# Performance work log

Hardware: AMD Instinct MI355X
Metric: run time of the kernel (lower is better)

The kernel has to match this reference:

```python
import jax, jax.numpy as jnp
import numpy as np

B, N, D = 8, 1024, 512
H = 8
DH = D // H
EPS_DIST = 1e-8
EPS_LN = 1e-5


def _layer_norm(x, gamma, beta):
    mu = jnp.mean(x, axis=-1, keepdims=True)
    var = jnp.mean((x - mu) ** 2, axis=-1, keepdims=True)
    return (x - mu) * jax.lax.rsqrt(var + EPS_LN) * gamma + beta


def setup_inputs() -> dict:
    key = jax.random.key(0)
    ks = jax.random.split(key, 6)
    scale = 1.0 / np.sqrt(D)
    inp = {
        "x": jax.random.normal(ks[0], (B, N, D), dtype=jnp.float32),
        "Wq": jax.random.normal(ks[1], (D, D), dtype=jnp.float32) * scale,
        "Wk": jax.random.normal(ks[2], (D, D), dtype=jnp.float32) * scale,
        "Wv": jax.random.normal(ks[3], (D, D), dtype=jnp.float32) * scale,
        "Wo": jax.random.normal(ks[4], (D, D), dtype=jnp.float32) * scale,
        "bq": jnp.zeros((D,), jnp.float32),
        "bk": jnp.zeros((D,), jnp.float32),
        "bv": jnp.zeros((D,), jnp.float32),
        "bo": jnp.zeros((D,), jnp.float32),
        "ln1_g": jnp.ones((D,), jnp.float32),
        "ln1_b": jnp.zeros((D,), jnp.float32),
        "ln2_g": jnp.ones((D,), jnp.float32),
        "ln2_b": jnp.zeros((D,), jnp.float32),
    }
    return inp


def reference(x, Wq, bq, Wk, bk, Wv, bv, Wo, bo, ln1_g, ln1_b, ln2_g, ln2_b):
    residual = x
    h = _layer_norm(x, ln1_g, ln1_b)  # pre-norm

    def heads(t):
        # [B,N,D] -> [B,H,N,DH]
        return t.reshape(B, N, H, DH).transpose(0, 2, 1, 3)

    q = heads(h @ Wq + bq)
    k = heads(h @ Wk + bk)
    v = heads(h @ Wv + bv)

    # Euclidean pairwise distance via ||q||^2 + ||k||^2 - 2 q.k expansion
    q_sq = jnp.sum(q * q, axis=-1)[..., :, None]      # [B,H,N,1]
    k_sq = jnp.sum(k * k, axis=-1)[..., None, :]      # [B,H,1,N]
    qk = jnp.einsum("bhnd,bhmd->bhnm", q, k)          # [B,H,N,N]
    d2 = jnp.maximum(q_sq + k_sq - 2.0 * qk, 0.0)
    dist = jnp.sqrt(d2 + EPS_DIST)

    # distance -> attention score: smaller distance = higher attention
    attn = jax.nn.softmax(-dist, axis=-1)             # [B,H,N,N]

    out = jnp.einsum("bhnm,bhmd->bhnd", attn, v)      # [B,H,N,DH]
    out = out.transpose(0, 2, 1, 3).reshape(B, N, D)
    out = out @ Wo + bo

    y = residual + out
    y = _layer_norm(y, ln2_g, ln2_b)
    return y
```

## Files before the change

kernel.cpp:

```cpp
#include <hip/hip_runtime.h>
#include <math.h>

typedef __attribute__((ext_vector_type(8))) short short8;
typedef __attribute__((ext_vector_type(4))) float f32x4;

constexpr int B  = 8;
constexpr int N  = 1024;
constexpr int D  = 512;
constexpr int H  = 8;
constexpr int DH = 64;
constexpr int M_ROWS = 8192;
constexpr float EPS_DIST = 1e-8f;
constexpr float EPS_LN   = 1e-5f;

__device__ inline unsigned short bfbits(float f) {
    union { float f; unsigned u; } v; v.f = f;
    unsigned r = v.u + 0x7fffu + ((v.u >> 16) & 1u);
    return (unsigned short)(r >> 16);
}
__device__ inline float bf2f(unsigned short s) {
    union { unsigned u; float f; } v; v.u = ((unsigned)s) << 16; return v.f;
}

__device__ inline int swz(int row) {
    return (((row >> 2) & 3) << 4) ^ ((row & 3) << 3);
}

__device__ inline void async_ld16(unsigned short* lds, const unsigned short* g) {
    __builtin_amdgcn_global_load_lds(
        (const __attribute__((address_space(1))) unsigned int*)(g),
        (__attribute__((address_space(3))) unsigned int*)(lds),
        16, 0, 0);
}

__device__ inline float block_sum256(float s, float* red) {
    for (int o = 32; o > 0; o >>= 1) s += __shfl_down(s, o, 64);
    int lane = threadIdx.x & 63, wid = threadIdx.x >> 6;
    if (lane == 0) red[wid] = s;
    __syncthreads();
    if (threadIdx.x == 0) red[4] = red[0] + red[1] + red[2] + red[3];
    __syncthreads();
    return red[4];
}

__global__ __launch_bounds__(256) void prep_kernel(const float* __restrict__ Wq,
                                                   const float* __restrict__ Wk,
                                                   const float* __restrict__ Wv,
                                                   const float* __restrict__ Wo,
                                                   unsigned short* __restrict__ WtAll,
                                                   const float* __restrict__ x,
                                                   const float* __restrict__ ln1_g,
                                                   const float* __restrict__ ln1_b,
                                                   unsigned short* __restrict__ h_bf) {
    __shared__ float red[8];
    const int bxg = blockIdx.x;
    if (bxg < 256) {
        int sub = bxg >> 6;
        const float* W = sub == 0 ? Wq : sub == 1 ? Wk : sub == 2 ? Wv : Wo;
        unsigned short* Wt = WtAll + (size_t)sub * 262144;
        int t = (bxg & 63) * 256 + threadIdx.x;
        int tn = t & 127, tk = t >> 7;
        int k = tk * 4, n = tn * 4;
        float4 r0 = *(const float4*)&W[(size_t)(k + 0) * 512 + n];
        float4 r1 = *(const float4*)&W[(size_t)(k + 1) * 512 + n];
        float4 r2 = *(const float4*)&W[(size_t)(k + 2) * 512 + n];
        float4 r3 = *(const float4*)&W[(size_t)(k + 3) * 512 + n];
        ushort4 c;
        c.x = bfbits(r0.x); c.y = bfbits(r1.x); c.z = bfbits(r2.x); c.w = bfbits(r3.x);
        *(ushort4*)&Wt[(size_t)(n + 0) * 512 + k] = c;
        c.x = bfbits(r0.y); c.y = bfbits(r1.y); c.z = bfbits(r2.y); c.w = bfbits(r3.y);
        *(ushort4*)&Wt[(size_t)(n + 1) * 512 + k] = c;
        c.x = bfbits(r0.z); c.y = bfbits(r1.z); c.z = bfbits(r2.z); c.w = bfbits(r3.z);
        *(ushort4*)&Wt[(size_t)(n + 2) * 512 + k] = c;
        c.x = bfbits(r0.w); c.y = bfbits(r1.w); c.z = bfbits(r2.w); c.w = bfbits(r3.w);
        *(ushort4*)&Wt[(size_t)(n + 3) * 512 + k] = c;
    } else {
        const int row = bxg - 256;
        const int t = threadIdx.x;
        const float* xr = x + (size_t)row * D;
        float v0 = xr[t], v1 = xr[t + 256];
        float mu = block_sum256(v0 + v1, red) * (1.0f / D);
        float d0 = v0 - mu, d1 = v1 - mu;
        float var = block_sum256(d0 * d0 + d1 * d1, red) * (1.0f / D);
        float rstd = rsqrtf(var + EPS_LN);
        h_bf[(size_t)row * D + t]       = bfbits(d0 * rstd * ln1_g[t] + ln1_b[t]);
        h_bf[(size_t)row * D + t + 256] = bfbits(d1 * rstd * ln1_g[t + 256] + ln1_b[t + 256]);
    }
}

__global__ __launch_bounds__(256) void ln2_kernel(const unsigned short* __restrict__ y0,
                                                  const float* __restrict__ res,
                                                  const float* __restrict__ gamma,
                                                  const float* __restrict__ beta,
                                                  float* __restrict__ out) {
    __shared__ float red[8];
    const int row = blockIdx.x;
    const int t = threadIdx.x;
    const unsigned short* xr = y0 + (size_t)row * D;
    const float* rr = res + (size_t)row * D;
    float v0 = bf2f(xr[t]) + rr[t];
    float v1 = bf2f(xr[t + 256]) + rr[t + 256];
    float mu = block_sum256(v0 + v1, red) * (1.0f / D);
    float d0 = v0 - mu, d1 = v1 - mu;
    float var = block_sum256(d0 * d0 + d1 * d1, red) * (1.0f / D);
    float rstd = rsqrtf(var + EPS_LN);
    out[(size_t)row * D + t]       = d0 * rstd * gamma[t] + beta[t];
    out[(size_t)row * D + t + 256] = d1 * rstd * gamma[t + 256] + beta[t + 256];
}

template <int MT>
__global__ __launch_bounds__(256) void gemm_qkv(const unsigned short* __restrict__ A,
                                                const unsigned short* __restrict__ Wt,
                                                const float* __restrict__ bias0,
                                                const float* __restrict__ bias1,
                                                const float* __restrict__ bias2,
                                                unsigned short* __restrict__ Qo,
                                                unsigned short* __restrict__ Ko,
                                                unsigned short* __restrict__ Vo,
                                                float* __restrict__ sq0,
                                                float* __restrict__ sq1) {
    constexpr int RB = M_ROWS / MT;
    constexpr int NI = MT / 32;
    constexpr int ASZ = MT * 64, BSZ = 128 * 64;
    constexpr int SMSZ = (ASZ + BSZ > 18432) ? ASZ + BSZ : 18432;
    __shared__ unsigned short smem[SMSZ];
    unsigned short* As = smem;
    unsigned short* Bs = smem + ASZ;

    const int id = blockIdx.x;
    const int by = id & (RB - 1), bx = id / RB;
    const int tid = threadIdx.x;
    const int lane = tid & 63, wv = tid >> 6;
    const int quad = lane >> 4, l15 = lane & 15;
    const int row0 = by * MT, col0 = bx * 128;
    const int wm = (wv & 1) * (MT / 2), wn = (wv >> 1) * 64;

    f32x4 acc[NI][4];
    #pragma unroll
    for (int i = 0; i < NI; ++i)
        #pragma unroll
        for (int j = 0; j < 4; ++j) acc[i][j] = (f32x4){0.f, 0.f, 0.f, 0.f};

    const unsigned short* Ag = A  + (size_t)row0 * 512;
    const unsigned short* Bg = Wt + (size_t)col0 * 512;

    for (int k0 = 0; k0 < 512; k0 += 64) {
        __syncthreads();
        #pragma unroll
        for (int c = 0; c < ASZ / 2048; ++c) {
            int fu = c * 2048 + tid * 8;
            int r = fu >> 6, ko = fu & 63;
            async_ld16(As + fu, Ag + (size_t)r * 512 + k0 + ko);
        }
        #pragma unroll
        for (int c = 0; c < BSZ / 2048; ++c) {
            int fu = c * 2048 + tid * 8;
            int r = fu >> 6, ko = fu & 63;
            async_ld16(Bs + fu, Bg + (size_t)r * 512 + k0 + ko);
        }
        __syncthreads();

        #pragma unroll
        for (int ks = 0; ks < 2; ++ks) {
            short8 af[NI], bf[4];
            #pragma unroll
            for (int i = 0; i < NI; ++i)
                af[i] = *(const short8*)&As[(wm + i * 16 + l15) * 64 + ks * 32 + quad * 8];
            #pragma unroll
            for (int j = 0; j < 4; ++j)
                bf[j] = *(const short8*)&Bs[(wn + j * 16 + l15) * 64 + ks * 32 + quad * 8];
            #pragma unroll
            for (int i = 0; i < NI; ++i)
                #pragma unroll
                for (int j = 0; j < 4; ++j)
                    acc[i][j] = __builtin_amdgcn_mfma_f32_16x16x32_bf16(af[i], bf[j], acc[i][j], 0, 0, 0);
        }
    }

    const int colg = col0 + wn;
    const int seg = colg >> 9;
    const int hh = (colg & 511) >> 6;
    const float* bias = seg == 0 ? bias0 : seg == 1 ? bias1 : bias2;

    if (seg < 2) {
        unsigned short* dst = seg == 0 ? Qo : Ko;
        float* sq = seg == 0 ? sq0 : sq1;
        #pragma unroll
        for (int i = 0; i < NI; ++i) {
            const int m0 = row0 + wm + i * 16 + quad * 4;
            float ss[4] = {0.f, 0.f, 0.f, 0.f};
            #pragma unroll
            for (int j = 0; j < 4; ++j) {
                float bvj = bias[hh * 64 + j * 16 + l15];
                #pragma unroll
                for (int r = 0; r < 4; ++r) {
                    float v = acc[i][j][r] + bvj;
                    unsigned short ub = bfbits(v);
                    float vr = bf2f(ub);
                    ss[r] += vr * vr;
                    int m = m0 + r;
                    int b_ = m >> 10, n_ = m & 1023;
                    dst[((size_t)((b_ * 8 + hh) * 1024) + n_) * 64 + j * 16 + l15] = ub;
                }
            }
            #pragma unroll
            for (int r = 0; r < 4; ++r) {
                float s = ss[r];
                s += __shfl_xor(s, 1, 64);
                s += __shfl_xor(s, 2, 64);
                s += __shfl_xor(s, 4, 64);
                s += __shfl_xor(s, 8, 64);
                if (l15 == 0) {
                    int m = m0 + r;
                    sq[(size_t)((m >> 10) * 8 + hh) * 1024 + (m & 1023)] = s;
                }
            }
        }
    } else {
        __syncthreads();
        unsigned short* T = smem + wv * 4608;
        #pragma unroll
        for (int i = 0; i < NI; ++i)
            #pragma unroll
            for (int j = 0; j < 4; ++j) {
                float bvj = bias[hh * 64 + j * 16 + l15];
                ushort4 pk;
                pk.x = bfbits(acc[i][j][0] + bvj);
                pk.y = bfbits(acc[i][j][1] + bvj);
                pk.z = bfbits(acc[i][j][2] + bvj);
                pk.w = bfbits(acc[i][j][3] + bvj);
                *(ushort4*)&T[(j * 16 + l15) * 72 + i * 16 + quad * 4] = pk;
            }
        const int b_ = (row0 + wm) >> 10;
        const int nbase = (row0 + wm) & 1023;
        unsigned short* Vg = Vo + ((size_t)((b_ * 8 + hh) * 64)) * 1024 + nbase;
        #pragma unroll
        for (int it = 0; it < 8; ++it) {
            int dl = it * 8 + (lane >> 3);
            int nl = (lane & 7) * 8;
            uint4 v = *(const uint4*)&T[dl * 72 + nl];
            *(uint4*)&Vg[(size_t)dl * 1024 + nl] = v;
        }
    }
}

__global__ __launch_bounds__(256) void gemm_out(const unsigned short* __restrict__ A,
                                                const unsigned short* __restrict__ Wt,
                                                const float* __restrict__ bias,
                                                unsigned short* __restrict__ C) {
    __shared__ unsigned short As[64 * 64];
    __shared__ unsigned short Bs[128 * 64];

    const int id = blockIdx.x;
    const int by = id & 127, bx = id >> 7;
    const int tid = threadIdx.x;
    const int lane = tid & 63, wv = tid >> 6;
    const int quad = lane >> 4, l15 = lane & 15;
    const int row0 = by * 64, col0 = bx * 128;
    const int wm = (wv & 1) * 32, wn = (wv >> 1) * 64;

    f32x4 acc[2][4];
    #pragma unroll
    for (int i = 0; i < 2; ++i)
        #pragma unroll
        for (int j = 0; j < 4; ++j) acc[i][j] = (f32x4){0.f, 0.f, 0.f, 0.f};

    const unsigned short* Ag = A  + (size_t)row0 * 512;
    const unsigned short* Bg = Wt + (size_t)col0 * 512;

    for (int k0 = 0; k0 < 512; k0 += 64) {
        __syncthreads();
        #pragma unroll
        for (int c = 0; c < 2; ++c) {
            int fu = c * 2048 + tid * 8;
            int r = fu >> 6, ko = fu & 63;
            async_ld16(As + fu, Ag + (size_t)r * 512 + k0 + ko);
        }
        #pragma unroll
        for (int c = 0; c < 4; ++c) {
            int fu = c * 2048 + tid * 8;
            int r = fu >> 6, ko = fu & 63;
            async_ld16(Bs + fu, Bg + (size_t)r * 512 + k0 + ko);
        }
        __syncthreads();

        #pragma unroll
        for (int ks = 0; ks < 2; ++ks) {
            short8 af[2], bf[4];
            #pragma unroll
            for (int i = 0; i < 2; ++i)
                af[i] = *(const short8*)&As[(wm + i * 16 + l15) * 64 + ks * 32 + quad * 8];
            #pragma unroll
            for (int j = 0; j < 4; ++j)
                bf[j] = *(const short8*)&Bs[(wn + j * 16 + l15) * 64 + ks * 32 + quad * 8];
            #pragma unroll
            for (int i = 0; i < 2; ++i)
                #pragma unroll
                for (int j = 0; j < 4; ++j)
                    acc[i][j] = __builtin_amdgcn_mfma_f32_16x16x32_bf16(af[i], bf[j], acc[i][j], 0, 0, 0);
        }
    }

    #pragma unroll
    for (int i = 0; i < 2; ++i)
        #pragma unroll
        for (int j = 0; j < 4; ++j) {
            int col = col0 + wn + j * 16 + l15;
            float bv = bias[col];
            #pragma unroll
            for (int r = 0; r < 4; ++r) {
                int row = row0 + wm + i * 16 + quad * 4 + r;
                C[(size_t)row * 512 + col] = bfbits(acc[i][j][r] + bv);
            }
        }
}

__global__ __launch_bounds__(512) void attn_kernel(const unsigned short* __restrict__ Q,
                                                   const unsigned short* __restrict__ K,
                                                   const unsigned short* __restrict__ Vt,
                                                   const float* __restrict__ qsq,
                                                   const float* __restrict__ ksq,
                                                   unsigned short* __restrict__ O) {
    __shared__ unsigned short Ks[2][64 * 64];
    __shared__ unsigned short Vs[2][64 * 64];
    __shared__ unsigned short Ps[8][16 * 64];
    __shared__ float ksq_s[2][64];

    const int id = blockIdx.x;
    const int bh = id & 63, qb = id >> 6;
    const int q0 = qb * 128;
    const int tid = threadIdx.x;
    const int lane = tid & 63, w = tid >> 6;
    const int quad = lane >> 4, l15 = lane & 15;
    const int b_ = bh >> 3, h_ = bh & 7;

    const unsigned short* Qb = Q  + (size_t)bh * N * DH;
    const unsigned short* Kb = K  + (size_t)bh * N * DH;
    const unsigned short* Vb = Vt + (size_t)bh * DH * N;

    short8 qf0, qf1;
    {
        const unsigned short* qp = Qb + (size_t)(q0 + w * 16 + l15) * 64 + quad * 8;
        qf0 = *(const short8*)qp;
        qf1 = *(const short8*)(qp + 32);
    }
    float qe[4];
    #pragma unroll
    for (int r = 0; r < 4; ++r)
        qe[r] = qsq[bh * N + q0 + w * 16 + quad * 4 + r] + EPS_DIST;

    f32x4 oacc[4];
    #pragma unroll
    for (int dt = 0; dt < 4; ++dt) oacc[dt] = (f32x4){0.f, 0.f, 0.f, 0.f};
    float dpart[4] = {};

    const int rr = tid >> 3;
    const int scol = ((tid & 7) * 8) ^ swz(rr);
    uint4 kreg, vreg;
    float ksreg = 0.f;

    kreg = *(const uint4*)(Kb + (size_t)rr * 64 + (tid & 7) * 8);
    vreg = *(const uint4*)(Vb + (size_t)rr * N + (tid & 7) * 8);
    if (tid < 64) ksreg = ksq[bh * N + tid];

    *(uint4*)&Ks[0][rr * 64 + scol] = kreg;
    *(uint4*)&Vs[0][rr * 64 + scol] = vreg;
    if (tid < 64) ksq_s[0][tid] = ksreg;
    __syncthreads();

    const int sR = swz(l15);

    #pragma unroll 2
    for (int kt = 0; kt < 16; ++kt) {
        const int cur = kt & 1;
        if (kt < 15) {
            kreg = *(const uint4*)(Kb + (size_t)((kt + 1) * 64 + rr) * 64 + (tid & 7) * 8);
            vreg = *(const uint4*)(Vb + (size_t)rr * N + (kt + 1) * 64 + (tid & 7) * 8);
            if (tid < 64) ksreg = ksq[bh * N + (kt + 1) * 64 + tid];
        }

        #pragma unroll
        for (int kb = 0; kb < 4; ++kb) {
            const int krow = kb * 16 + l15;
            short8 kf0 = *(const short8*)&Ks[cur][krow * 64 + ((quad * 8) ^ sR)];
            short8 kf1 = *(const short8*)&Ks[cur][krow * 64 + ((32 + quad * 8) ^ sR)];
            float ks2 = ksq_s[cur][kb * 16 + l15];
            f32x4 sa = (f32x4){0.f, 0.f, 0.f, 0.f};
            sa = __builtin_amdgcn_mfma_f32_16x16x32_bf16(qf0, kf0, sa, 0, 0, 0);
            sa = __builtin_amdgcn_mfma_f32_16x16x32_bf16(qf1, kf1, sa, 0, 0, 0);
            #pragma unroll
            for (int r = 0; r < 4; ++r) {
                float d2 = fmaf(-2.0f, sa[r], qe[r] + ks2);
                d2 = fmaxf(d2, EPS_DIST);
                float p = __expf(-__builtin_amdgcn_sqrtf(d2));
                dpart[r] += p;
                union { float f; unsigned u; } pu; pu.f = p;
                const int prow = quad * 4 + r;
                Ps[w][prow * 64 + ((kb * 16 + l15) ^ swz(prow))] =
                    (unsigned short)(pu.u >> 16);
            }
        }

        short8 vf[4][2];
        #pragma unroll
        for (int dt = 0; dt < 4; ++dt) {
            const int vrow = dt * 16 + l15;
            #pragma unroll
            for (int kc = 0; kc < 2; ++kc)
                vf[dt][kc] = *(const short8*)&Vs[cur][vrow * 64 + ((kc * 32 + quad * 8) ^ sR)];
        }
        #pragma unroll
        for (int kc = 0; kc < 2; ++kc) {
            short8 pf = *(const short8*)&Ps[w][l15 * 64 + ((kc * 32 + quad * 8) ^ sR)];
            #pragma unroll
            for (int dt = 0; dt < 4; ++dt)
                oacc[dt] = __builtin_amdgcn_mfma_f32_16x16x32_bf16(pf, vf[dt][kc], oacc[dt], 0, 0, 0);
        }

        if (kt < 15) {
            *(uint4*)&Ks[cur ^ 1][rr * 64 + scol] = kreg;
            *(uint4*)&Vs[cur ^ 1][rr * 64 + scol] = vreg;
            if (tid < 64) ksq_s[cur ^ 1][tid] = ksreg;
        }
        __syncthreads();
    }

    float rinv[4];
    #pragma unroll
    for (int r = 0; r < 4; ++r) {
        float s = dpart[r];
        s += __shfl_xor(s, 1, 64);
        s += __shfl_xor(s, 2, 64);
        s += __shfl_xor(s, 4, 64);
        s += __shfl_xor(s, 8, 64);
        rinv[r] = 1.0f / s;
    }

    #pragma unroll
    for (int dt = 0; dt < 4; ++dt)
        #pragma unroll
        for (int r = 0; r < 4; ++r) {
            int n_ = q0 + w * 16 + quad * 4 + r;
            O[((size_t)(b_ * N + n_) * D) + h_ * DH + dt * 16 + l15] =
                bfbits(oacc[dt][r] * rinv[r]);
        }
}

extern "C" void kernel_launch(void* const* d_in, const int* in_sizes, int n_in,
                              void* d_out, int out_size, void* d_ws, size_t ws_size,
                              hipStream_t stream) {
    const float* x     = (const float*)d_in[0];
    const float* Wq    = (const float*)d_in[1];
    const float* Wk    = (const float*)d_in[2];
    const float* Wv    = (const float*)d_in[3];
    const float* Wo    = (const float*)d_in[4];
    const float* bq    = (const float*)d_in[5];
    const float* bk    = (const float*)d_in[6];
    const float* bv    = (const float*)d_in[7];
    const float* bo    = (const float*)d_in[8];
    const float* ln1_g = (const float*)d_in[9];
    const float* ln1_b = (const float*)d_in[10];
    const float* ln2_g = (const float*)d_in[11];
    const float* ln2_b = (const float*)d_in[12];
    float* out = (float*)d_out;

    unsigned short* WtAll = (unsigned short*)d_ws;
    unsigned short* h_bf  = WtAll + 4 * 262144;
    unsigned short* Qb    = h_bf + 4194304;
    unsigned short* Kb    = Qb + 4194304;
    unsigned short* Vtg   = Kb + 4194304;
    unsigned short* Ob    = Vtg + 4194304;
    unsigned short* Y0    = Ob + 4194304;
    float* qsq = (float*)(Y0 + 4194304);
    float* ksq = qsq + 65536;

    prep_kernel<<<256 + M_ROWS, 256, 0, stream>>>(Wq, Wk, Wv, Wo, WtAll,
                                                  x, ln1_g, ln1_b, h_bf);

    gemm_qkv<128><<<768, 256, 0, stream>>>(h_bf, WtAll, bq, bk, bv,
                                           Qb, Kb, Vtg, qsq, ksq);

    attn_kernel<<<512, 512, 0, stream>>>(Qb, Kb, Vtg, qsq, ksq, Ob);

    gemm_out<<<512, 256, 0, stream>>>(Ob, WtAll + 3 * 262144, bo, Y0);

    ln2_kernel<<<M_ROWS, 256, 0, stream>>>(Y0, x, ln2_g, ln2_b, out);
}
```

Measured before the change: 188.6 us.

## Shrink attention blocks to 64 queries, pad LDS rows, single-buffer K/V tiles

The attention kernel now runs 1024 blocks of 256 threads, each covering 64 queries instead of 128. The XOR-swizzled, double-buffered K/V/P shared-memory tiles are replaced by single-buffered tiles padded to 72 columns, so each tile needs two barriers per iteration. The change aims to raise block count and occupancy and to simplify LDS addressing. In exchange, every block loads each K/V tile for half as many queries, so global K/V traffic doubles, and the extra barrier may expose load latency.

```diff
diff --git a/kernel.cpp b/kernel.cpp
--- a/kernel.cpp
+++ b/kernel.cpp
@@ -20,10 +20,6 @@
 }
 __device__ inline float bf2f(unsigned short s) {
     union { unsigned u; float f; } v; v.u = ((unsigned)s) << 16; return v.f;
-}
-
-__device__ inline int swz(int row) {
-    return (((row >> 2) & 3) << 4) ^ ((row & 3) << 3);
 }
 
 __device__ inline void async_ld16(unsigned short* lds, const unsigned short* g) {
@@ -315,20 +311,20 @@
         }
 }
 
-__global__ __launch_bounds__(512) void attn_kernel(const unsigned short* __restrict__ Q,
+__global__ __launch_bounds__(256) void attn_kernel(const unsigned short* __restrict__ Q,
                                                    const unsigned short* __restrict__ K,
                                                    const unsigned short* __restrict__ Vt,
                                                    const float* __restrict__ qsq,
                                                    const float* __restrict__ ksq,
                                                    unsigned short* __restrict__ O) {
-    __shared__ unsigned short Ks[2][64 * 64];
-    __shared__ unsigned short Vs[2][64 * 64];
-    __shared__ unsigned short Ps[8][16 * 64];
-    __shared__ float ksq_s[2][64];
+    __shared__ unsigned short Ks[64][72];
+    __shared__ unsigned short Vs[64][72];
+    __shared__ unsigned short Ps[4][16][72];
+    __shared__ float ksq_s[64];
 
     const int id = blockIdx.x;
     const int bh = id & 63, qb = id >> 6;
-    const int q0 = qb * 128;
+    const int q0 = qb * 64;
     const int tid = threadIdx.x;
     const int lane = tid & 63, w = tid >> 6;
     const int quad = lane >> 4, l15 = lane & 15;
@@ -354,37 +350,37 @@
     for (int dt = 0; dt < 4; ++dt) oacc[dt] = (f32x4){0.f, 0.f, 0.f, 0.f};
     float dpart[4] = {};
 
-    const int rr = tid >> 3;
-    const int scol = ((tid & 7) * 8) ^ swz(rr);
-    uint4 kreg, vreg;
+    const int rr = tid >> 2, cc = (tid & 3) * 16;
+    uint4 kreg0, kreg1, vreg0, vreg1;
     float ksreg = 0.f;
 
-    kreg = *(const uint4*)(Kb + (size_t)rr * 64 + (tid & 7) * 8);
-    vreg = *(const uint4*)(Vb + (size_t)rr * N + (tid & 7) * 8);
+    kreg0 = *(const uint4*)(Kb + (size_t)rr * 64 + cc);
+    kreg1 = *(const uint4*)(Kb + (size_t)rr * 64 + cc + 8);
+    vreg0 = *(const uint4*)(Vb + (size_t)rr * N + cc);
+    vreg1 = *(const uint4*)(Vb + (size_t)rr * N + cc + 8);
     if (tid < 64) ksreg = ksq[bh * N + tid];
 
-    *(uint4*)&Ks[0][rr * 64 + scol] = kreg;
-    *(uint4*)&Vs[0][rr * 64 + scol] = vreg;
-    if (tid < 64) ksq_s[0][tid] = ksreg;
+    *(uint4*)&Ks[rr][cc]     = kreg0;
+    *(uint4*)&Ks[rr][cc + 8] = kreg1;
+    *(uint4*)&Vs[rr][cc]     = vreg0;
+    *(uint4*)&Vs[rr][cc + 8] = vreg1;
+    if (tid < 64) ksq_s[tid] = ksreg;
     __syncthreads();
 
-    const int sR = swz(l15);
-
-    #pragma unroll 2
     for (int kt = 0; kt < 16; ++kt) {
-        const int cur = kt & 1;
         if (kt < 15) {
-            kreg = *(const uint4*)(Kb + (size_t)((kt + 1) * 64 + rr) * 64 + (tid & 7) * 8);
-            vreg = *(const uint4*)(Vb + (size_t)rr * N + (kt + 1) * 64 + (tid & 7) * 8);
+            kreg0 = *(const uint4*)(Kb + (size_t)((kt + 1) * 64 + rr) * 64 + cc);
+            kreg1 = *(const uint4*)(Kb + (size_t)((kt + 1) * 64 + rr) * 64 + cc + 8);
+            vreg0 = *(const uint4*)(Vb + (size_t)rr * N + (kt + 1) * 64 + cc);
+            vreg1 = *(const uint4*)(Vb + (size_t)rr * N + (kt + 1) * 64 + cc + 8);
             if (tid < 64) ksreg = ksq[bh * N + (kt + 1) * 64 + tid];
         }
 
         #pragma unroll
         for (int kb = 0; kb < 4; ++kb) {
-            const int krow = kb * 16 + l15;
-            short8 kf0 = *(const short8*)&Ks[cur][krow * 64 + ((quad * 8) ^ sR)];
-            short8 kf1 = *(const short8*)&Ks[cur][krow * 64 + ((32 + quad * 8) ^ sR)];
-            float ks2 = ksq_s[cur][kb * 16 + l15];
+            short8 kf0 = *(const short8*)&Ks[kb * 16 + l15][quad * 8];
+            short8 kf1 = *(const short8*)&Ks[kb * 16 + l15][32 + quad * 8];
+            float ks2 = ksq_s[kb * 16 + l15];
             f32x4 sa = (f32x4){0.f, 0.f, 0.f, 0.f};
             sa = __builtin_amdgcn_mfma_f32_16x16x32_bf16(qf0, kf0, sa, 0, 0, 0);
             sa = __builtin_amdgcn_mfma_f32_16x16x32_bf16(qf1, kf1, sa, 0, 0, 0);
@@ -395,34 +391,33 @@
                 float p = __expf(-__builtin_amdgcn_sqrtf(d2));
                 dpart[r] += p;
                 union { float f; unsigned u; } pu; pu.f = p;
-                const int prow = quad * 4 + r;
-                Ps[w][prow * 64 + ((kb * 16 + l15) ^ swz(prow))] =
-                    (unsigned short)(pu.u >> 16);
+                Ps[w][quad * 4 + r][kb * 16 + l15] = (unsigned short)(pu.u >> 16);
             }
         }
 
         short8 vf[4][2];
         #pragma unroll
-        for (int dt = 0; dt < 4; ++dt) {
-            const int vrow = dt * 16 + l15;
+        for (int dt = 0; dt < 4; ++dt)
             #pragma unroll
             for (int kc = 0; kc < 2; ++kc)
-                vf[dt][kc] = *(const short8*)&Vs[cur][vrow * 64 + ((kc * 32 + quad * 8) ^ sR)];
-        }
+                vf[dt][kc] = *(const short8*)&Vs[dt * 16 + l15][kc * 32 + quad * 8];
         #pragma unroll
         for (int kc = 0; kc < 2; ++kc) {
-            short8 pf = *(const short8*)&Ps[w][l15 * 64 + ((kc * 32 + quad * 8) ^ sR)];
+            short8 pf = *(const short8*)&Ps[w][l15][kc * 32 + quad * 8];
             #pragma unroll
             for (int dt = 0; dt < 4; ++dt)
                 oacc[dt] = __builtin_amdgcn_mfma_f32_16x16x32_bf16(pf, vf[dt][kc], oacc[dt], 0, 0, 0);
         }
 
         if (kt < 15) {
-            *(uint4*)&Ks[cur ^ 1][rr * 64 + scol] = kreg;
-            *(uint4*)&Vs[cur ^ 1][rr * 64 + scol] = vreg;
-            if (tid < 64) ksq_s[cur ^ 1][tid] = ksreg;
-        }
-        __syncthreads();
+            __syncthreads();
+            *(uint4*)&Ks[rr][cc]     = kreg0;
+            *(uint4*)&Ks[rr][cc + 8] = kreg1;
+            *(uint4*)&Vs[rr][cc]     = vreg0;
+            *(uint4*)&Vs[rr][cc + 8] = vreg1;
+            if (tid < 64) ksq_s[tid] = ksreg;
+            __syncthreads();
+        }
     }
 
     float rinv[4];
@@ -480,7 +475,7 @@
     gemm_qkv<128><<<768, 256, 0, stream>>>(h_bf, WtAll, bq, bk, bv,
                                            Qb, Kb, Vtg, qsq, ksq);
 
-    attn_kernel<<<512, 512, 0, stream>>>(Qb, Kb, Vtg, qsq, ksq, Ob);
+    attn_kernel<<<1024, 256, 0, stream>>>(Qb, Kb, Vtg, qsq, ksq, Ob);
 
     gemm_out<<<512, 256, 0, stream>>>(Ob, WtAll + 3 * 262144, bo, Y0);
 
```

Result: no change. 186.9 us (-0.9%).
